# Performance work log

Measured on AMD Instinct MI355X. Metric: run time of the kernel, lower is better.

## Reference

```python
import jax, jax.numpy as jnp
import numpy as np

INPUT_DIM = 128
HIDDEN = 512
FEAT = 256


def setup_inputs() -> dict:
    key = jax.random.key(0)
    ks = jax.random.split(key, 9)
    B, T, D, H, F = 1024, 256, INPUT_DIM, HIDDEN, FEAT
    s_ih = 1.0 / np.sqrt(H)
    return {
        "isequence": jax.random.normal(ks[0], (B, T, D), dtype=jnp.float32),
        "W_ih": jax.random.uniform(ks[1], (4 * H, D), jnp.float32, -s_ih, s_ih),
        "W_hh": jax.random.uniform(ks[2], (4 * H, H), jnp.float32, -s_ih, s_ih),
        "b_ih": jax.random.uniform(ks[3], (4 * H,), jnp.float32, -s_ih, s_ih),
        "b_hh": jax.random.uniform(ks[4], (4 * H,), jnp.float32, -s_ih, s_ih),
        "W_feat": jax.random.uniform(ks[5], (F, H), jnp.float32, -s_ih, s_ih),
        "b_feat": jax.random.uniform(ks[6], (F,), jnp.float32, -s_ih, s_ih),
        "W_out": jax.random.uniform(ks[7], (2, F), jnp.float32, -1.0 / np.sqrt(F), 1.0 / np.sqrt(F)),
        "b_out": jax.random.uniform(ks[8], (2,), jnp.float32, -1.0 / np.sqrt(F), 1.0 / np.sqrt(F)),
    }


def reference(isequence, W_ih, W_hh, b_ih, b_hh, W_feat, b_feat, W_out, b_out):
    B, T, D = isequence.shape
    H = W_hh.shape[1]
    # Precompute input projections for all timesteps: [T, B, 4H]
    x_t = jnp.transpose(isequence, (1, 0, 2))  # time-major [T, B, D]
    x_proj = jnp.einsum('tbd,gd->tbg', x_t, W_ih) + b_ih + b_hh

    def step(carry, xp):
        h, c = carry
        gates = xp + h @ W_hh.T  # [B, 4H]
        i, f, g, o = jnp.split(gates, 4, axis=-1)  # torch LSTMCell gate order
        i = jax.nn.sigmoid(i)
        f = jax.nn.sigmoid(f)
        g = jnp.tanh(g)
        o = jax.nn.sigmoid(o)
        c_new = f * c + i * g
        h_new = o * jnp.tanh(c_new)
        return (h_new, c_new), None

    h0 = jnp.zeros((B, H), dtype=isequence.dtype)
    c0 = jnp.zeros((B, H), dtype=isequence.dtype)
    (h_T, _), _ = jax.lax.scan(step, (h0, c0), x_proj)
    features = h_T @ W_feat.T + b_feat
    return features @ W_out.T + b_out
```

## Files before the change

kernel.cpp:

```cpp
#include <hip/hip_runtime.h>

typedef _Float16 h16;
typedef __attribute__((ext_vector_type(8))) _Float16 half8;
typedef __attribute__((ext_vector_type(4))) float f32x4;
typedef __attribute__((ext_vector_type(4))) unsigned u32x4;
typedef unsigned long long ull;

#define B_   1024
#define T_   256
#define D_   128
#define H_   512
#define Kc_  640
#define NR_  2048
#define AGENT_ __HIP_MEMORY_SCOPE_AGENT

__device__ __forceinline__ float sigm_(float v) {
    return 1.0f / (1.0f + __expf(-v));
}
__device__ __forceinline__ float tanh_(float v) {
    v = fminf(15.0f, fmaxf(-15.0f, v));
    const float e = __expf(2.0f * v);
    return (e - 1.0f) / (e + 1.0f);
}

__global__ void prep_kernel(const float* __restrict__ Wih, const float* __restrict__ Whh,
                            const float* __restrict__ bih, const float* __restrict__ bhh,
                            h16* __restrict__ Wr, float* __restrict__ biasr,
                            unsigned* __restrict__ flags) {
    int idx = blockIdx.x * 256 + threadIdx.x;
    if (idx < NR_ * Kc_) {
        int R = idx / Kc_, k = idx - R * Kc_;
        int Q = R >> 4, rw = R & 15;
        int j = Q * 4 + (rw >> 2), q = rw & 3;
        int src = q * H_ + j;
        float w = (k < D_) ? Wih[src * D_ + k] : Whh[src * H_ + (k - D_)];
        Wr[idx] = (h16)w;
    }
    if (idx < NR_) {
        int Q = idx >> 4, rw = idx & 15;
        int j = Q * 4 + (rw >> 2), q = rw & 3;
        int src = q * H_ + j;
        biasr[idx] = bih[src] + bhh[src];
    }
    if (idx < 16384)
        __hip_atomic_store(flags + idx, 0u, __ATOMIC_RELAXED, AGENT_);
}

#define LOADW(dst, base) \
    asm volatile( \
        "global_load_dwordx4 %0, %20, off\n\t" \
        "global_load_dwordx4 %1, %20, off offset:64\n\t" \
        "global_load_dwordx4 %2, %20, off offset:128\n\t" \
        "global_load_dwordx4 %3, %20, off offset:192\n\t" \
        "global_load_dwordx4 %4, %20, off offset:256\n\t" \
        "global_load_dwordx4 %5, %20, off offset:320\n\t" \
        "global_load_dwordx4 %6, %20, off offset:384\n\t" \
        "global_load_dwordx4 %7, %20, off offset:448\n\t" \
        "global_load_dwordx4 %8, %20, off offset:512\n\t" \
        "global_load_dwordx4 %9, %20, off offset:576\n\t" \
        "global_load_dwordx4 %10, %20, off offset:640\n\t" \
        "global_load_dwordx4 %11, %20, off offset:704\n\t" \
        "global_load_dwordx4 %12, %20, off offset:768\n\t" \
        "global_load_dwordx4 %13, %20, off offset:832\n\t" \
        "global_load_dwordx4 %14, %20, off offset:896\n\t" \
        "global_load_dwordx4 %15, %20, off offset:960\n\t" \
        "global_load_dwordx4 %16, %20, off offset:1024\n\t" \
        "global_load_dwordx4 %17, %20, off offset:1088\n\t" \
        "global_load_dwordx4 %18, %20, off offset:1152\n\t" \
        "global_load_dwordx4 %19, %20, off offset:1216\n\t" \
        "s_waitcnt vmcnt(0)" \
        : "=&v"(dst[0]), "=&v"(dst[1]), "=&v"(dst[2]), "=&v"(dst[3]), \
          "=&v"(dst[4]), "=&v"(dst[5]), "=&v"(dst[6]), "=&v"(dst[7]), \
          "=&v"(dst[8]), "=&v"(dst[9]), "=&v"(dst[10]), "=&v"(dst[11]), \
          "=&v"(dst[12]), "=&v"(dst[13]), "=&v"(dst[14]), "=&v"(dst[15]), \
          "=&v"(dst[16]), "=&v"(dst[17]), "=&v"(dst[18]), "=&v"(dst[19]) \
        : "v"(base))

__global__ void __launch_bounds__(512, 2) lstm_kernel(
    const float* __restrict__ x,
    const h16*  __restrict__ Wr,
    const float* __restrict__ biasr,
    h16* __restrict__ hbuf,
    unsigned* __restrict__ flags)
{
    __shared__ __align__(16) char ldsx[8192];
    __shared__ __align__(16) char ldshA[16384];
    __shared__ __align__(16) char ldshB[16384];
    __shared__ __align__(16) char ldsb[2048];

    const int blk = blockIdx.x;
    const int bt  = blk >> 3;
    const int ht  = blk & 7;
    const int tid = threadIdx.x;
    const int wv  = tid >> 6, l = tid & 63;
    const int ll  = l & 15, lh = l >> 4;
    const int Rb  = ht * 256 + wv * 32;
    const int bbase = bt * 32;

    half8 warr0[20], warr1[20];
    {
        const h16* wb0 = Wr + (size_t)(Rb + ll) * Kc_ + lh * 8;
        const h16* wb1 = Wr + (size_t)(Rb + 16 + ll) * Kc_ + lh * 8;
        LOADW(warr0, wb0);
        LOADW(warr1, wb1);
    }
    f32x4 bias4[2];
    bias4[0] = *reinterpret_cast<const f32x4*>(biasr + Rb + lh * 4);
    bias4[1] = *reinterpret_cast<const f32x4*>(biasr + Rb + 16 + lh * 4);

    float cstA[2] = {0.f, 0.f}, cstB[2] = {0.f, 0.f};

    const int xrow = tid >> 4, xcol = tid & 15;
    const int hrow = tid >> 5, hcol = tid & 31;

    unsigned* fbase = flags + bt * 512;
    unsigned* myfA  = fbase + ht * 32;
    unsigned* myfB  = fbase + 256 + ht * 32;
    const unsigned* wfpA = fbase + (l & 7) * 32;
    const unsigned* wfpB = fbase + 256 + (l & 7) * 32;

    unsigned fv = 0;
    f32x4 xv0, xv1;
    u32x4 hv0, hv1;

    auto issueFlag = [&](const unsigned* p) {
        asm volatile("global_load_dword %0, %1, off sc0 sc1" : "=v"(fv) : "v"(p));
    };
    auto issueX = [&](int t) {
        const float* xp = x + ((size_t)(bbase + xrow) * T_ + t) * D_ + xcol * 8;
        asm volatile("global_load_dwordx4 %0, %2, off\n\t"
                     "global_load_dwordx4 %1, %2, off offset:16"
                     : "=&v"(xv0), "=&v"(xv1) : "v"(xp));
    };
    auto issueH = [&](const h16* hsrc, int rowoff) {
        const char* hp = (const char*)(hsrc + (size_t)(bbase + rowoff + hrow) * H_) + hcol * 32;
        asm volatile("global_load_dwordx4 %0, %2, off sc0 sc1\n\t"
                     "global_load_dwordx4 %1, %2, off offset:16 sc0 sc1"
                     : "=&v"(hv0), "=&v"(hv1) : "v"(hp) : "memory");
    };
    auto spinFlag = [&](unsigned tgt, const unsigned* p) {
        while (!__all(fv >= tgt)) {
            __builtin_amdgcn_s_sleep(2);
            asm volatile("global_load_dword %0, %1, off sc0 sc1\n\ts_waitcnt vmcnt(0)"
                         : "=v"(fv) : "v"(p) : "memory");
        }
    };
    auto stageX = [&]() {
        half8 r;
#pragma unroll
        for (int u = 0; u < 4; ++u) { r[u] = (h16)xv0[u]; r[4 + u] = (h16)xv1[u]; }
        *reinterpret_cast<half8*>(ldsx + ((xrow * 256 + xcol * 16) ^ ((xrow & 7) << 4))) = r;
    };
    auto stageH = [&](char* ldsh) {
        const int swz = (hrow & 7) << 4;
        const int g0 = hcol * 2, g1 = hcol * 2 + 1;
        *reinterpret_cast<u32x4*>(ldsh + ((hrow * 1024 + (g0 ^ (g0 >> 1)) * 16) ^ swz)) = hv0;
        *reinterpret_cast<u32x4*>(ldsh + ((hrow * 1024 + (g1 ^ (g1 >> 1)) * 16) ^ swz)) = hv1;
    };
    auto computeX = [&](int rowoff, f32x4* acc) {
#pragma unroll
        for (int kk = 0; kk < 4; ++kk) {
            const int row = rowoff + ll;
            half8 bf = *reinterpret_cast<const half8*>(
                ldsx + ((row * 256 + (kk * 4 + lh) * 16) ^ ((row & 7) << 4)));
            acc[0] = __builtin_amdgcn_mfma_f32_16x16x32_f16(warr0[kk], bf, acc[0], 0, 0, 0);
            acc[1] = __builtin_amdgcn_mfma_f32_16x16x32_f16(warr1[kk], bf, acc[1], 0, 0, 0);
        }
    };
    auto computeH_lo = [&](const char* ldsh, f32x4* acc) {
#pragma unroll
        for (int kk = 0; kk < 8; ++kk) {
            const int ks = kk * 4 + lh;
            half8 bf = *reinterpret_cast<const half8*>(
                ldsh + ((ll * 1024 + (ks ^ (ks >> 1)) * 16) ^ ((ll & 7) << 4)));
            acc[0] = __builtin_amdgcn_mfma_f32_16x16x32_f16(warr0[4 + kk], bf, acc[0], 0, 0, 0);
            acc[1] = __builtin_amdgcn_mfma_f32_16x16x32_f16(warr1[4 + kk], bf, acc[1], 0, 0, 0);
        }
    };
    auto computeH_hi = [&](const char* ldsh, f32x4* acc) {
#pragma unroll
        for (int kk = 8; kk < 16; ++kk) {
            const int ks = kk * 4 + lh;
            half8 bf = *reinterpret_cast<const half8*>(
                ldsh + ((ll * 1024 + (ks ^ (ks >> 1)) * 16) ^ ((ll & 7) << 4)));
            acc[0] = __builtin_amdgcn_mfma_f32_16x16x32_f16(warr0[4 + kk], bf, acc[0], 0, 0, 0);
            acc[1] = __builtin_amdgcn_mfma_f32_16x16x32_f16(warr1[4 + kk], bf, acc[1], 0, 0, 0);
        }
    };
    auto cellHalf = [&](f32x4* acc, float* cst) {
#pragma unroll
        for (int rt = 0; rt < 2; ++rt) {
            f32x4 g4 = acc[rt];
            const float gi = sigm_(g4[0]);
            const float gf = sigm_(g4[1]);
            const float gg = tanh_(g4[2]);
            const float go = sigm_(g4[3]);
            const float c  = gf * cst[rt] + gi * gg;
            cst[rt] = c;
            const float hn = go * tanh_(c);
            const int u = wv * 8 + rt * 4 + lh;
            *reinterpret_cast<h16*>(ldsb + ((ll * 128 + u * 2) ^ ((ll & 7) << 4))) = (h16)hn;
        }
    };
    auto storeHalf = [&](h16* hcur, int rowoff) {
        if (tid < 256) {
            const int r2 = tid >> 4, c2 = tid & 15;
            ull pk = *reinterpret_cast<const ull*>(
                ldsb + ((r2 * 128 + c2 * 8) ^ ((r2 & 7) << 4)));
            ull* dst = reinterpret_cast<ull*>(
                hcur + (size_t)(bbase + rowoff + r2) * H_ + ht * 64 + c2 * 4);
            __hip_atomic_store(dst, pk, __ATOMIC_RELAXED, AGENT_);
        }
    };

    {
        half8 z;
#pragma unroll
        for (int u = 0; u < 8; ++u) z[u] = (h16)0.f;
        *reinterpret_cast<half8*>(ldshA + tid * 32)      = z;
        *reinterpret_cast<half8*>(ldshA + tid * 32 + 16) = z;
        *reinterpret_cast<half8*>(ldshB + tid * 32)      = z;
        *reinterpret_cast<half8*>(ldshB + tid * 32 + 16) = z;
        issueX(0);
        asm volatile("s_waitcnt vmcnt(0)" : "+v"(xv0), "+v"(xv1) :: "memory");
        stageX();
    }
    __syncthreads();

    for (int t = 0; t < T_; ++t) {
        h16* hcur        = hbuf + (size_t)(t & 1) * (B_ * H_);
        const h16* hprev = hbuf + (size_t)((t & 1) ^ 1) * (B_ * H_);

        if (t > 0) issueFlag(wfpB);
        issueX(t + 1 < T_ ? t + 1 : t);
        f32x4 acc[2] = {bias4[0], bias4[1]};
        computeX(0, acc);
        computeH_lo(ldshA, acc);
        if (t > 0) {
            asm volatile("s_waitcnt vmcnt(2)" : "+v"(fv) :: "memory");
            if (!__all(fv >= (unsigned)t)) spinFlag((unsigned)t, wfpB);
            issueH(hprev, 16);
        }
        computeH_hi(ldshA, acc);
        cellHalf(acc, cstA);
        __syncthreads();
        if (t > 0) {
            asm volatile("s_waitcnt vmcnt(0)" : "+v"(hv0), "+v"(hv1) :: "memory");
            stageH(ldshB);
        }
        storeHalf(hcur, 0);
        __syncthreads();
        if (tid == 0)
            __hip_atomic_store(myfA, (unsigned)(t + 1), __ATOMIC_RELAXED, AGENT_);

        issueFlag(wfpA);
        f32x4 accB[2] = {bias4[0], bias4[1]};
        computeX(16, accB);
        computeH_lo(ldshB, accB);
        asm volatile("s_waitcnt vmcnt(0)" : "+v"(fv) :: "memory");
        if (!__all(fv >= (unsigned)(t + 1))) spinFlag((unsigned)(t + 1), wfpA);
        issueH(hcur, 0);
        computeH_hi(ldshB, accB);
        cellHalf(accB, cstB);
        __syncthreads();
        asm volatile("s_waitcnt vmcnt(0)"
                     : "+v"(hv0), "+v"(hv1), "+v"(xv0), "+v"(xv1) :: "memory");
        stageH(ldshA);
        stageX();
        storeHalf(hcur, 16);
        __syncthreads();
        if (tid == 0)
            __hip_atomic_store(myfB, (unsigned)(t + 1), __ATOMIC_RELAXED, AGENT_);
    }
}

__global__ void __launch_bounds__(256) final_kernel(
    const h16* __restrict__ hT, const float* __restrict__ Wfeat,
    const float* __restrict__ bfeat, const float* __restrict__ Wout,
    const float* __restrict__ bout, float* __restrict__ out)
{
    __shared__ __align__(16) h16 hsh[16][512];
    __shared__ float fsh[16][256];
    const int tid = threadIdx.x;
    const int b0  = blockIdx.x * 16;

    {
        const int row = tid >> 4, seg = tid & 15;
        const half8* s8 = reinterpret_cast<const half8*>(hT + (size_t)(b0 + row) * H_ + seg * 32);
        half8* d8 = reinterpret_cast<half8*>(&hsh[row][seg * 32]);
        d8[0] = s8[0]; d8[1] = s8[1]; d8[2] = s8[2]; d8[3] = s8[3];
    }
    __syncthreads();

    float acc[16];
#pragma unroll
    for (int b = 0; b < 16; ++b) acc[b] = 0.f;
    const float* wrow = Wfeat + (size_t)tid * H_;
    for (int k8 = 0; k8 < H_ / 8; ++k8) {
        f32x4 w0 = *reinterpret_cast<const f32x4*>(wrow + k8 * 8);
        f32x4 w1 = *reinterpret_cast<const f32x4*>(wrow + k8 * 8 + 4);
#pragma unroll
        for (int b = 0; b < 16; ++b) {
            half8 h8 = *reinterpret_cast<const half8*>(&hsh[b][k8 * 8]);
#pragma unroll
            for (int u = 0; u < 4; ++u) {
                acc[b] = fmaf(w0[u], (float)h8[u], acc[b]);
                acc[b] = fmaf(w1[u], (float)h8[4 + u], acc[b]);
            }
        }
    }
    const float bf = bfeat[tid];
#pragma unroll
    for (int b = 0; b < 16; ++b) fsh[b][tid] = acc[b] + bf;
    __syncthreads();

    if (tid < 32) {
        const int b = tid >> 1, oc = tid & 1;
        float a = bout[oc];
        const float* wo = Wout + oc * 256;
        for (int f = 0; f < 256; ++f) a = fmaf(wo[f], fsh[b][f], a);
        out[(size_t)(b0 + b) * 2 + oc] = a;
    }
}

extern "C" void kernel_launch(void* const* d_in, const int* in_sizes, int n_in,
                              void* d_out, int out_size, void* d_ws, size_t ws_size,
                              hipStream_t stream) {
    const float* x     = (const float*)d_in[0];
    const float* Wih   = (const float*)d_in[1];
    const float* Whh   = (const float*)d_in[2];
    const float* bih   = (const float*)d_in[3];
    const float* bhh   = (const float*)d_in[4];
    const float* Wfeat = (const float*)d_in[5];
    const float* bfeat = (const float*)d_in[6];
    const float* Wout  = (const float*)d_in[7];
    const float* bout  = (const float*)d_in[8];
    float* out = (float*)d_out;

    char* ws = (char*)d_ws;
    h16*      Wr    = (h16*)ws;
    float*    biasr = (float*)(ws + 2621440);
    h16*      hbuf  = (h16*)(ws + 2621440 + 8192);
    unsigned* flags = (unsigned*)(ws + 2621440 + 8192 + 2097152);

    prep_kernel<<<dim3((NR_ * Kc_ + 255) / 256), dim3(256), 0, stream>>>(
        Wih, Whh, bih, bhh, Wr, biasr, flags);

    void* args[] = {(void*)&x, (void*)&Wr, (void*)&biasr, (void*)&hbuf, (void*)&flags};
    hipLaunchCooperativeKernel((void*)lstm_kernel, dim3(256), dim3(512), args, 0, stream);

    const h16* hT = hbuf + (size_t)(B_ * H_);
    final_kernel<<<dim3(B_ / 16), dim3(256), 0, stream>>>(hT, Wfeat, bfeat, Wout, bout, out);
}
```

Baseline: 1.184 ms.

## Use per-wave completion flags and drop a block barrier per half-step

Each wave now writes its own slice of h straight from a private LDS stripe and raises its own flag, instead of the whole block staging h, syncing, storing, syncing, then thread 0 flagging. Consumers poll 64 per-wave flags per lane rather than 8 per-block flags. This removes one __syncthreads per half-step and shortens the critical path from cell compute to flag publication. In exchange there are more flag writes and wider polling, and H compute is no longer split around the spin wait, so less MFMA work overlaps the wait.

```diff
diff --git a/kernel.cpp b/kernel.cpp
--- a/kernel.cpp
+++ b/kernel.cpp
@@ -113,18 +113,26 @@
     const int xrow = tid >> 4, xcol = tid & 15;
     const int hrow = tid >> 5, hcol = tid & 31;
 
-    unsigned* fbase = flags + bt * 512;
-    unsigned* myfA  = fbase + ht * 32;
-    unsigned* myfB  = fbase + 256 + ht * 32;
-    const unsigned* wfpA = fbase + (l & 7) * 32;
-    const unsigned* wfpB = fbase + 256 + (l & 7) * 32;
+    unsigned* fbase = flags + bt * 128;
+    unsigned* myfA  = fbase + (ht * 8 + wv);
+    unsigned* myfB  = fbase + 64 + (ht * 8 + wv);
+    const unsigned* pollA = fbase + l;
+    const unsigned* pollB = fbase + 64 + l;
 
     unsigned fv = 0;
-    f32x4 xv0, xv1;
-    u32x4 hv0, hv1;
-
-    auto issueFlag = [&](const unsigned* p) {
+    f32x4 xv0 = {0, 0, 0, 0}, xv1 = {0, 0, 0, 0};
+    u32x4 hv0 = {0, 0, 0, 0}, hv1 = {0, 0, 0, 0};
+
+    auto issuePoll = [&](const unsigned* p) {
         asm volatile("global_load_dword %0, %1, off sc0 sc1" : "=v"(fv) : "v"(p));
+    };
+    auto waitSpin = [&](unsigned tgt, const unsigned* p) {
+        asm volatile("s_waitcnt vmcnt(0)" : "+v"(fv) :: "memory");
+        while (!__all(fv >= tgt)) {
+            __builtin_amdgcn_s_sleep(2);
+            asm volatile("global_load_dword %0, %1, off sc0 sc1\n\ts_waitcnt vmcnt(0)"
+                         : "=v"(fv) : "v"(p) : "memory");
+        }
     };
     auto issueX = [&](int t) {
         const float* xp = x + ((size_t)(bbase + xrow) * T_ + t) * D_ + xcol * 8;
@@ -137,13 +145,6 @@
         asm volatile("global_load_dwordx4 %0, %2, off sc0 sc1\n\t"
                      "global_load_dwordx4 %1, %2, off offset:16 sc0 sc1"
                      : "=&v"(hv0), "=&v"(hv1) : "v"(hp) : "memory");
-    };
-    auto spinFlag = [&](unsigned tgt, const unsigned* p) {
-        while (!__all(fv >= tgt)) {
-            __builtin_amdgcn_s_sleep(2);
-            asm volatile("global_load_dword %0, %1, off sc0 sc1\n\ts_waitcnt vmcnt(0)"
-                         : "=v"(fv) : "v"(p) : "memory");
-        }
     };
     auto stageX = [&]() {
         half8 r;
@@ -167,9 +168,9 @@
             acc[1] = __builtin_amdgcn_mfma_f32_16x16x32_f16(warr1[kk], bf, acc[1], 0, 0, 0);
         }
     };
-    auto computeH_lo = [&](const char* ldsh, f32x4* acc) {
-#pragma unroll
-        for (int kk = 0; kk < 8; ++kk) {
+    auto computeH = [&](const char* ldsh, f32x4* acc) {
+#pragma unroll
+        for (int kk = 0; kk < 16; ++kk) {
             const int ks = kk * 4 + lh;
             half8 bf = *reinterpret_cast<const half8*>(
                 ldsh + ((ll * 1024 + (ks ^ (ks >> 1)) * 16) ^ ((ll & 7) << 4)));
@@ -177,17 +178,9 @@
             acc[1] = __builtin_amdgcn_mfma_f32_16x16x32_f16(warr1[4 + kk], bf, acc[1], 0, 0, 0);
         }
     };
-    auto computeH_hi = [&](const char* ldsh, f32x4* acc) {
-#pragma unroll
-        for (int kk = 8; kk < 16; ++kk) {
-            const int ks = kk * 4 + lh;
-            half8 bf = *reinterpret_cast<const half8*>(
-                ldsh + ((ll * 1024 + (ks ^ (ks >> 1)) * 16) ^ ((ll & 7) << 4)));
-            acc[0] = __builtin_amdgcn_mfma_f32_16x16x32_f16(warr0[4 + kk], bf, acc[0], 0, 0, 0);
-            acc[1] = __builtin_amdgcn_mfma_f32_16x16x32_f16(warr1[4 + kk], bf, acc[1], 0, 0, 0);
-        }
-    };
-    auto cellHalf = [&](f32x4* acc, float* cst) {
+    auto cellStoreFlag = [&](f32x4* acc, float* cst, h16* hcur, int rowoff,
+                             unsigned* myf, unsigned tval) {
+        char* stripe = ldsb + wv * 256;
 #pragma unroll
         for (int rt = 0; rt < 2; ++rt) {
             f32x4 g4 = acc[rt];
@@ -198,19 +191,19 @@
             const float c  = gf * cst[rt] + gi * gg;
             cst[rt] = c;
             const float hn = go * tanh_(c);
-            const int u = wv * 8 + rt * 4 + lh;
-            *reinterpret_cast<h16*>(ldsb + ((ll * 128 + u * 2) ^ ((ll & 7) << 4))) = (h16)hn;
-        }
-    };
-    auto storeHalf = [&](h16* hcur, int rowoff) {
-        if (tid < 256) {
-            const int r2 = tid >> 4, c2 = tid & 15;
-            ull pk = *reinterpret_cast<const ull*>(
-                ldsb + ((r2 * 128 + c2 * 8) ^ ((r2 & 7) << 4)));
-            ull* dst = reinterpret_cast<ull*>(
-                hcur + (size_t)(bbase + rowoff + r2) * H_ + ht * 64 + c2 * 4);
-            __hip_atomic_store(dst, pk, __ATOMIC_RELAXED, AGENT_);
-        }
+            *reinterpret_cast<h16*>(stripe + ll * 16 + (rt * 4 + lh) * 2) = (h16)hn;
+        }
+        asm volatile("s_waitcnt lgkmcnt(0)" ::: "memory");
+        __builtin_amdgcn_sched_barrier(0);
+        const unsigned pk = *reinterpret_cast<const unsigned*>(
+            stripe + (l >> 2) * 16 + (l & 3) * 4);
+        unsigned* dst = reinterpret_cast<unsigned*>(
+            hcur + (size_t)(bbase + rowoff + (l >> 2)) * H_ + ht * 64 + wv * 8 + (l & 3) * 2);
+        __hip_atomic_store(dst, pk, __ATOMIC_RELAXED, AGENT_);
+        asm volatile("s_waitcnt vmcnt(0)"
+                     : "+v"(hv0), "+v"(hv1), "+v"(xv0), "+v"(xv1) :: "memory");
+        if (l == 0)
+            __hip_atomic_store(myf, tval, __ATOMIC_RELAXED, AGENT_);
     };
 
     {
@@ -231,46 +224,32 @@
         h16* hcur        = hbuf + (size_t)(t & 1) * (B_ * H_);
         const h16* hprev = hbuf + (size_t)((t & 1) ^ 1) * (B_ * H_);
 
-        if (t > 0) issueFlag(wfpB);
-        issueX(t + 1 < T_ ? t + 1 : t);
+        if (t > 0) issuePoll(pollB);
         f32x4 acc[2] = {bias4[0], bias4[1]};
         computeX(0, acc);
-        computeH_lo(ldshA, acc);
         if (t > 0) {
-            asm volatile("s_waitcnt vmcnt(2)" : "+v"(fv) :: "memory");
-            if (!__all(fv >= (unsigned)t)) spinFlag((unsigned)t, wfpB);
+            waitSpin((unsigned)t, pollB);
             issueH(hprev, 16);
         }
-        computeH_hi(ldshA, acc);
-        cellHalf(acc, cstA);
+        issueX(t + 1 < T_ ? t + 1 : t);
+        computeH(ldshA, acc);
+        cellStoreFlag(acc, cstA, hcur, 0, myfA, (unsigned)(t + 1));
+        if (t > 0) stageH(ldshB);
         __syncthreads();
-        if (t > 0) {
-            asm volatile("s_waitcnt vmcnt(0)" : "+v"(hv0), "+v"(hv1) :: "memory");
-            stageH(ldshB);
-        }
-        storeHalf(hcur, 0);
-        __syncthreads();
-        if (tid == 0)
-            __hip_atomic_store(myfA, (unsigned)(t + 1), __ATOMIC_RELAXED, AGENT_);
-
-        issueFlag(wfpA);
+
+        const int more = (t + 1 < T_);
+        if (more) issuePoll(pollA);
         f32x4 accB[2] = {bias4[0], bias4[1]};
         computeX(16, accB);
-        computeH_lo(ldshB, accB);
-        asm volatile("s_waitcnt vmcnt(0)" : "+v"(fv) :: "memory");
-        if (!__all(fv >= (unsigned)(t + 1))) spinFlag((unsigned)(t + 1), wfpA);
-        issueH(hcur, 0);
-        computeH_hi(ldshB, accB);
-        cellHalf(accB, cstB);
+        if (more) {
+            waitSpin((unsigned)(t + 1), pollA);
+            issueH(hcur, 0);
+        }
+        computeH(ldshB, accB);
+        cellStoreFlag(accB, cstB, hcur, 16, myfB, (unsigned)(t + 1));
+        if (more) stageH(ldshA);
+        stageX();
         __syncthreads();
-        asm volatile("s_waitcnt vmcnt(0)"
-                     : "+v"(hv0), "+v"(hv1), "+v"(xv0), "+v"(xv1) :: "memory");
-        stageH(ldshA);
-        stageX();
-        storeHalf(hcur, 16);
-        __syncthreads();
-        if (tid == 0)
-            __hip_atomic_store(myfB, (unsigned)(t + 1), __ATOMIC_RELAXED, AGENT_);
     }
 }
 
```

Result: slower. 1.569 ms (+32.6%).

## Use per-wave completion flags and LDS-only barriers in persistent LSTM loop

Applied to the files above, without the earlier changes.

Replaces the single per-block flag, published by thread 0 after a full __syncthreads, with per-wave flags. Each storing wave drains its own vmcnt and then publishes, and pollers read 32 flags per batch tile across lanes. The __syncthreads calls become a lgkmcnt-only wait plus s_barrier, which avoids waiting on outstanding global loads at barriers. The x prefetch moves after the first half, and the spin sleep is shortened. This risks more flag traffic and depends on per-wave store ordering for correctness.

```diff
diff --git a/kernel.cpp b/kernel.cpp
--- a/kernel.cpp
+++ b/kernel.cpp
@@ -13,6 +13,8 @@
 #define Kc_  640
 #define NR_  2048
 #define AGENT_ __HIP_MEMORY_SCOPE_AGENT
+
+#define LBAR() asm volatile("s_waitcnt lgkmcnt(0)\n\ts_barrier" ::: "memory")
 
 __device__ __forceinline__ float sigm_(float v) {
     return 1.0f / (1.0f + __expf(-v));
@@ -113,18 +115,24 @@
     const int xrow = tid >> 4, xcol = tid & 15;
     const int hrow = tid >> 5, hcol = tid & 31;
 
-    unsigned* fbase = flags + bt * 512;
-    unsigned* myfA  = fbase + ht * 32;
-    unsigned* myfB  = fbase + 256 + ht * 32;
-    const unsigned* wfpA = fbase + (l & 7) * 32;
-    const unsigned* wfpB = fbase + 256 + (l & 7) * 32;
+    unsigned* myfA = flags + bt * 32 + ht * 4 + wv;
+    unsigned* myfB = flags + 1024 + bt * 32 + ht * 4 + wv;
+    const unsigned* pollA = flags + bt * 32 + (l & 31);
+    const unsigned* pollB = flags + 1024 + bt * 32 + (l & 31);
 
     unsigned fv = 0;
     f32x4 xv0, xv1;
     u32x4 hv0, hv1;
 
-    auto issueFlag = [&](const unsigned* p) {
+    auto issuePoll = [&](const unsigned* p) {
         asm volatile("global_load_dword %0, %1, off sc0 sc1" : "=v"(fv) : "v"(p));
+    };
+    auto spinFlag = [&](unsigned tgt, const unsigned* p) {
+        while (!__all(fv >= tgt)) {
+            __builtin_amdgcn_s_sleep(1);
+            asm volatile("global_load_dword %0, %1, off sc0 sc1\n\ts_waitcnt vmcnt(0)"
+                         : "=v"(fv) : "v"(p) : "memory");
+        }
     };
     auto issueX = [&](int t) {
         const float* xp = x + ((size_t)(bbase + xrow) * T_ + t) * D_ + xcol * 8;
@@ -137,13 +145,6 @@
         asm volatile("global_load_dwordx4 %0, %2, off sc0 sc1\n\t"
                      "global_load_dwordx4 %1, %2, off offset:16 sc0 sc1"
                      : "=&v"(hv0), "=&v"(hv1) : "v"(hp) : "memory");
-    };
-    auto spinFlag = [&](unsigned tgt, const unsigned* p) {
-        while (!__all(fv >= tgt)) {
-            __builtin_amdgcn_s_sleep(2);
-            asm volatile("global_load_dword %0, %1, off sc0 sc1\n\ts_waitcnt vmcnt(0)"
-                         : "=v"(fv) : "v"(p) : "memory");
-        }
     };
     auto stageX = [&]() {
         half8 r;
@@ -212,6 +213,13 @@
             __hip_atomic_store(dst, pk, __ATOMIC_RELAXED, AGENT_);
         }
     };
+    auto drainFlag = [&](unsigned* myf, unsigned tval) {
+        if (tid < 256) {
+            asm volatile("s_waitcnt vmcnt(0)" ::: "memory");
+            if (l == 0)
+                __hip_atomic_store(myf, tval, __ATOMIC_RELAXED, AGENT_);
+        }
+    };
 
     {
         half8 z;
@@ -231,46 +239,44 @@
         h16* hcur        = hbuf + (size_t)(t & 1) * (B_ * H_);
         const h16* hprev = hbuf + (size_t)((t & 1) ^ 1) * (B_ * H_);
 
-        if (t > 0) issueFlag(wfpB);
-        issueX(t + 1 < T_ ? t + 1 : t);
+        if (t > 0) issuePoll(pollB);
         f32x4 acc[2] = {bias4[0], bias4[1]};
         computeX(0, acc);
         computeH_lo(ldshA, acc);
         if (t > 0) {
-            asm volatile("s_waitcnt vmcnt(2)" : "+v"(fv) :: "memory");
-            if (!__all(fv >= (unsigned)t)) spinFlag((unsigned)t, wfpB);
+            asm volatile("s_waitcnt vmcnt(0)" : "+v"(fv) :: "memory");
+            if (!__all(fv >= (unsigned)t)) spinFlag((unsigned)t, pollB);
             issueH(hprev, 16);
         }
         computeH_hi(ldshA, acc);
         cellHalf(acc, cstA);
-        __syncthreads();
+        LBAR();
         if (t > 0) {
             asm volatile("s_waitcnt vmcnt(0)" : "+v"(hv0), "+v"(hv1) :: "memory");
             stageH(ldshB);
         }
         storeHalf(hcur, 0);
-        __syncthreads();
-        if (tid == 0)
-            __hip_atomic_store(myfA, (unsigned)(t + 1), __ATOMIC_RELAXED, AGENT_);
-
-        issueFlag(wfpA);
+        LBAR();
+        drainFlag(myfA, (unsigned)(t + 1));
+
+        issuePoll(pollA);
+        issueX(t + 1 < T_ ? t + 1 : t);
         f32x4 accB[2] = {bias4[0], bias4[1]};
         computeX(16, accB);
         computeH_lo(ldshB, accB);
-        asm volatile("s_waitcnt vmcnt(0)" : "+v"(fv) :: "memory");
-        if (!__all(fv >= (unsigned)(t + 1))) spinFlag((unsigned)(t + 1), wfpA);
+        asm volatile("s_waitcnt vmcnt(2)" : "+v"(fv) :: "memory");
+        if (!__all(fv >= (unsigned)(t + 1))) spinFlag((unsigned)(t + 1), pollA);
         issueH(hcur, 0);
         computeH_hi(ldshB, accB);
         cellHalf(accB, cstB);
-        __syncthreads();
+        LBAR();
         asm volatile("s_waitcnt vmcnt(0)"
                      : "+v"(hv0), "+v"(hv1), "+v"(xv0), "+v"(xv1) :: "memory");
         stageH(ldshA);
         stageX();
         storeHalf(hcur, 16);
-        __syncthreads();
-        if (tid == 0)
-            __hip_atomic_store(myfB, (unsigned)(t + 1), __ATOMIC_RELAXED, AGENT_);
+        LBAR();
+        drainFlag(myfB, (unsigned)(t + 1));
     }
 }
 
```

After: 2.053 ms. +73.5%, slower.
